# Kernel optimization log

Hardware: AMD Instinct MI355X
Metric: run time of the kernel (lower is better)

The kernel has to match this reference:

```python
import jax, jax.numpy as jnp
import numpy as np

H = 512      # hidden_size
FF = 4 * H   # expert FFN inner dim
E = 8        # expert_num
K = 2        # top_k
B, S = 4, 4096


def setup_inputs() -> dict:
    key = jax.random.key(0)
    ks = jax.random.split(key, 4)
    s = 0.02
    return {
        "x":  jax.random.normal(ks[0], (B, S, H), dtype=jnp.float32),
        "Wg": jax.random.normal(ks[1], (H, E), dtype=jnp.float32) * s,
        "bg": jnp.zeros((E,), dtype=jnp.float32),
        "W1": jax.random.normal(ks[2], (E, H, FF), dtype=jnp.float32) * s,
        "b1": jnp.zeros((E, FF), dtype=jnp.float32),
        "W2": jax.random.normal(ks[3], (E, FF, H), dtype=jnp.float32) * s,
        "b2": jnp.zeros((E, H), dtype=jnp.float32),
    }


def reference(x, Wg, bg, W1, b1, W2, b2):
    # gate + top-k routing
    logits = x @ Wg + bg                               # [B,S,E]
    w, idx = jax.lax.top_k(logits, K)                  # [B,S,K]
    w = jax.nn.softmax(w, axis=-1)                     # softmax over top-k logits

    # naive dense MoE: every expert runs on every token (matches torch source)
    h = jax.nn.silu(jnp.einsum('bsh,ehf->ebsf', x, W1) + b1[:, None, None, :])  # [E,B,S,FF]
    y = jnp.einsum('ebsf,efh->ebsh', h, W2) + b2[:, None, None, :]              # [E,B,S,H]

    # one-hot mask * top-k weight, combined over slots (same math as torch loop)
    comb = jnp.einsum('bske,bsk->ebs', jax.nn.one_hot(idx, E, dtype=x.dtype), w)  # [E,B,S]
    return jnp.einsum('ebsh,ebs->bsh', y, comb)        # [B,S,H]
```

## Files before the change

### kernel.cpp

```cpp
#include <hip/hip_runtime.h>
#include <hip/hip_bf16.h>
#include <math.h>


#define T_TOK 16384
#define H_DIM 512
#define FF_DIM 2048
#define E_NUM 8
#define NSLOT (T_TOK * 2)
#define NB_ROUTE 128

typedef __attribute__((ext_vector_type(4))) float f32x4;
typedef __attribute__((ext_vector_type(8))) short s16x8;

__device__ __forceinline__ void gload_lds16(const void* g, void* l) {
    __builtin_amdgcn_global_load_lds((const __attribute__((address_space(1))) void*)g,
                                     (__attribute__((address_space(3))) void*)l, 16, 0, 0);
}

__device__ __forceinline__ unsigned short f2bf(float f) {
    union { float f; unsigned int u; } a; a.f = f;
    unsigned int r = a.u + 0x7FFF + ((a.u >> 16) & 1);
    return (unsigned short)(r >> 16);
}


__global__ __launch_bounds__(256) void zero_f32(float* p, int n) {
    int i = (blockIdx.x * 256 + threadIdx.x) * 4;
    if (i < n) { f32x4 z = {0.f, 0.f, 0.f, 0.f}; *(f32x4*)(p + i) = z; }
}

__global__ __launch_bounds__(256) void convert_x_bf16(const float* __restrict__ x,
                                                      unsigned short* __restrict__ xb) {
    int i = (blockIdx.x * 256 + threadIdx.x) * 8;
    f32x4 a = *(const f32x4*)(x + i);
    f32x4 b = *(const f32x4*)(x + i + 4);
    s16x8 o;
    o[0] = (short)f2bf(a[0]); o[1] = (short)f2bf(a[1]);
    o[2] = (short)f2bf(a[2]); o[3] = (short)f2bf(a[3]);
    o[4] = (short)f2bf(b[0]); o[5] = (short)f2bf(b[1]);
    o[6] = (short)f2bf(b[2]); o[7] = (short)f2bf(b[3]);
    *(s16x8*)(xb + i) = o;
}

__global__ __launch_bounds__(256) void transpose_bf16(const float* __restrict__ src,
                                                      unsigned short* __restrict__ dst,
                                                      int R, int C) {
    const int e = blockIdx.z;
    const int c0 = blockIdx.x * 32, r0 = blockIdx.y * 32;
    __shared__ float tile[32][33];
    const float* s = src + (size_t)e * R * C;
    unsigned short* d = dst + (size_t)e * R * C;
    const int tid = threadIdx.x;
    for (int idx = tid; idx < 1024; idx += 256) {
        int r = idx >> 5, c = idx & 31;
        tile[r][c] = s[(size_t)(r0 + r) * C + c0 + c];
    }
    __syncthreads();
    for (int idx = tid; idx < 1024; idx += 256) {
        int r = idx >> 5, c = idx & 31;
        d[(size_t)(c0 + r) * R + r0 + c] = f2bf(tile[c][r]);
    }
}


__global__ __launch_bounds__(256) void gate_topk(const float* __restrict__ x,
                                                 const float* __restrict__ Wg,
                                                 const float* __restrict__ bg,
                                                 int* __restrict__ eidx,
                                                 float* __restrict__ ewt) {
    const int t = blockIdx.x * 4 + (threadIdx.x >> 6);
    const int l = threadIdx.x & 63;
    const float* xr = x + (size_t)t * H_DIM;
    double part[E_NUM];
#pragma unroll
    for (int e = 0; e < E_NUM; ++e) part[e] = 0.0;
#pragma unroll
    for (int i = 0; i < 8; ++i) {
        const int h = l + 64 * i;
        const double xv = (double)xr[h];
        const float* wr = Wg + (size_t)h * E_NUM;
#pragma unroll
        for (int e = 0; e < E_NUM; ++e) part[e] += xv * (double)wr[e];
    }
    for (int s = 1; s < 64; s <<= 1) {
#pragma unroll
        for (int e = 0; e < E_NUM; ++e) part[e] += __shfl_xor(part[e], s);
    }
    if (l == 0) {
        double lg[E_NUM];
#pragma unroll
        for (int e = 0; e < E_NUM; ++e) lg[e] = part[e] + (double)bg[e];
        int e0 = 0;
        for (int e = 1; e < E_NUM; ++e) if (lg[e] > lg[e0]) e0 = e;
        int e1 = (e0 == 0) ? 1 : 0;
        for (int e = 0; e < E_NUM; ++e) if (e != e0 && lg[e] > lg[e1]) e1 = e;
        double z = exp(lg[e1] - lg[e0]);
        float w0 = (float)(1.0 / (1.0 + z));
        float w1 = (float)(z / (1.0 + z));
        eidx[2 * t] = e0; eidx[2 * t + 1] = e1;
        ewt[2 * t] = w0; ewt[2 * t + 1] = w1;
    }
}


__global__ __launch_bounds__(256) void count_blocks(const int* __restrict__ eidx,
                                                    int* __restrict__ blockcnt) {
    __shared__ int cnt[E_NUM];
    if (threadIdx.x < E_NUM) cnt[threadIdx.x] = 0;
    __syncthreads();
    const int s = blockIdx.x * 256 + threadIdx.x;
    atomicAdd(&cnt[eidx[s]], 1);
    __syncthreads();
    if (threadIdx.x < E_NUM)
        blockcnt[blockIdx.x * E_NUM + threadIdx.x] = cnt[threadIdx.x];
}

__global__ __launch_bounds__(512) void scan_blocks(const int* __restrict__ blockcnt,
                                                   int* __restrict__ bbase,
                                                   int* __restrict__ offsets) {
    __shared__ int tot[E_NUM];
    __shared__ int obase[E_NUM + 1];
    const int e = threadIdx.x >> 6;
    const int l = threadIdx.x & 63;
    const int a = blockcnt[(2 * l) * E_NUM + e];
    const int b = blockcnt[(2 * l + 1) * E_NUM + e];
    const int s = a + b;
    int sc = s;
    for (int d = 1; d < 64; d <<= 1) {
        int o = __shfl_up(sc, d);
        if (l >= d) sc += o;
    }
    const int excl = sc - s;
    if (l == 63) tot[e] = sc;
    __syncthreads();
    if (threadIdx.x == 0) {
        int acc = 0;
        for (int i = 0; i < E_NUM; ++i) { obase[i] = acc; acc += tot[i]; }
        obase[E_NUM] = acc;
        for (int i = 0; i <= E_NUM; ++i) offsets[i] = obase[i];
    }
    __syncthreads();
    const int base = obase[e] + excl;
    bbase[(2 * l) * E_NUM + e] = base;
    bbase[(2 * l + 1) * E_NUM + e] = base + a;
}

__global__ __launch_bounds__(256) void scatter_slots(const int* __restrict__ eidx,
                                                     const float* __restrict__ ewt,
                                                     const int* __restrict__ bbase,
                                                     int* __restrict__ slot_token,
                                                     float* __restrict__ slot_w,
                                                     int* __restrict__ slot_of) {
    __shared__ int cur[E_NUM];
    if (threadIdx.x < E_NUM)
        cur[threadIdx.x] = bbase[blockIdx.x * E_NUM + threadIdx.x];
    __syncthreads();
    const int s = blockIdx.x * 256 + threadIdx.x;
    const int e = eidx[s];
    const int pos = atomicAdd(&cur[e], 1);
    slot_token[pos] = s >> 1;
    slot_w[pos] = ewt[s];
    slot_of[s] = pos;
}


template<int EPI, int NT, int KD, int NTOT, int MC, int LDA>
__global__ __launch_bounds__(256, 3) void ggemm(
    const unsigned short* __restrict__ Ag,
    const unsigned short* __restrict__ Bt,
    const float* __restrict__ bias,
    const int* __restrict__ slot_token,
    const float* __restrict__ slot_w,
    const int* __restrict__ offsets,
    unsigned short* __restrict__ Hout,
    float* __restrict__ out) {
    const int e = blockIdx.x;
    const int nt = blockIdx.y % NT;
    const int mc = blockIdx.y / NT;
    const int base = offsets[e];
    const int cnt = offsets[e + 1] - base;
    if (cnt == 0) return;
    const int n0 = nt * 128;

    __shared__ __align__(16) unsigned short Abuf[128 * 64];
    __shared__ __align__(16) unsigned short Bbuf[128 * 64];

    const int tid = threadIdx.x;
    const int w = tid >> 6;
    const int l = tid & 63;
    const int wm = (w & 1) << 6;
    const int wn = (w >> 1) << 6;

    int aoff[4], boff[4];
#pragma unroll
    for (int i = 0; i < 4; ++i) {
        int r = wm + i * 16 + (l & 15);
        aoff[i] = r * 128 + ((((l >> 4) ^ (r & 7))) << 4);
    }
#pragma unroll
    for (int j = 0; j < 4; ++j) {
        int r = wn + j * 16 + (l & 15);
        boff[j] = r * 128 + ((((l >> 4) ^ (r & 7))) << 4);
    }

    const int srow = tid >> 3;
    const int sce = (tid & 7) * 8;
    const unsigned short* Bg = Bt + (size_t)e * NTOT * KD + (size_t)n0 * KD;
    const int nk = KD / 64;

    int bsrc[4];
#pragma unroll
    for (int p = 0; p < 4; ++p) {
        int row = p * 32 + srow;
        bsrc[p] = (row & ~63) | ((row & 15) << 2) | ((row >> 4) & 3);
    }

    for (int m0 = mc * 128; m0 < cnt; m0 += MC * 128) {
        int tokr[4];
#pragma unroll
        for (int p = 0; p < 4; ++p) {
            int s = m0 + p * 32 + srow;
            if (s > cnt - 1) s = cnt - 1;
            tokr[p] = (EPI == 0) ? slot_token[base + s] : (base + s);
        }

        f32x4 acc[4][4] = {};
        for (int kt = 0; kt < nk; ++kt) {
            const int k0 = kt * 64;
            __syncthreads();
#pragma unroll
            for (int p = 0; p < 4; ++p) {
                int row = p * 32 + srow;
                int ce = sce ^ ((row & 7) * 8);
                gload_lds16(Ag + (size_t)tokr[p] * LDA + k0 + ce, &Abuf[row * 64 + sce]);
                gload_lds16(Bg + (size_t)bsrc[p] * KD + k0 + ce, &Bbuf[row * 64 + sce]);
            }
            __syncthreads();
            const char* Ab = (const char*)&Abuf[0];
            const char* Bb = (const char*)&Bbuf[0];
#pragma unroll
            for (int half = 0; half < 2; ++half) {
                const int kb = half << 6;
                s16x8 af[4], bfv[4];
#pragma unroll
                for (int i = 0; i < 4; ++i) af[i] = *(const s16x8*)(Ab + (aoff[i] ^ kb));
#pragma unroll
                for (int j = 0; j < 4; ++j) bfv[j] = *(const s16x8*)(Bb + (boff[j] ^ kb));
#pragma unroll
                for (int i = 0; i < 4; ++i)
#pragma unroll
                    for (int j = 0; j < 4; ++j)
                        acc[i][j] = __builtin_amdgcn_mfma_f32_16x16x32_bf16(af[i], bfv[j], acc[i][j], 0, 0, 0);
            }
        }

        const int c0 = wn + (l & 15) * 4;
        float b4[4];
#pragma unroll
        for (int j = 0; j < 4; ++j) b4[j] = bias[(size_t)e * NTOT + n0 + c0 + j];

#pragma unroll
        for (int i = 0; i < 4; ++i) {
            const int rb = wm + i * 16 + ((l >> 4) << 2);
#pragma unroll
            for (int r = 0; r < 4; ++r) {
                const int row = m0 + rb + r;
                if (row >= cnt) continue;
                const int slot = base + row;
                if (EPI == 0) {
                    float v0 = acc[i][0][r] + b4[0];
                    float v1 = acc[i][1][r] + b4[1];
                    float v2 = acc[i][2][r] + b4[2];
                    float v3 = acc[i][3][r] + b4[3];
                    v0 = v0 / (1.0f + __expf(-v0));
                    v1 = v1 / (1.0f + __expf(-v1));
                    v2 = v2 / (1.0f + __expf(-v2));
                    v3 = v3 / (1.0f + __expf(-v3));
                    uint2 pk;
                    pk.x = (unsigned int)f2bf(v0) | ((unsigned int)f2bf(v1) << 16);
                    pk.y = (unsigned int)f2bf(v2) | ((unsigned int)f2bf(v3) << 16);
                    *(uint2*)&Hout[(size_t)slot * NTOT + n0 + c0] = pk;
                } else if (EPI == 2) {
                    const float wgt = slot_w[slot];
                    f32x4 v;
#pragma unroll
                    for (int j = 0; j < 4; ++j) v[j] = wgt * (acc[i][j][r] + b4[j]);
                    *(f32x4*)&out[(size_t)slot * NTOT + n0 + c0] = v;
                } else {
                    const int tok = slot_token[slot];
                    const float wgt = slot_w[slot];
                    float* op = out + (size_t)tok * NTOT + n0 + c0;
#pragma unroll
                    for (int j = 0; j < 4; ++j)
                        atomicAdd(op + j, wgt * (acc[i][j][r] + b4[j]));
                }
            }
        }
    }
}

__global__ __launch_bounds__(256) void combine_y(const float* __restrict__ Y,
                                                 const int* __restrict__ slot_of,
                                                 float* __restrict__ out) {
    const int idx = blockIdx.x * 256 + threadIdx.x;
    const int t = idx >> 6;
    const int h = (idx & 63) * 8;
    const int sa = slot_of[2 * t];
    const int sb = slot_of[2 * t + 1];
    const float* pa = Y + (size_t)sa * H_DIM + h;
    const float* pb = Y + (size_t)sb * H_DIM + h;
    f32x4 a0 = *(const f32x4*)pa, a1 = *(const f32x4*)(pa + 4);
    f32x4 b0 = *(const f32x4*)pb, b1 = *(const f32x4*)(pb + 4);
    float* po = out + (size_t)t * H_DIM + h;
    *(f32x4*)po = a0 + b0;
    *(f32x4*)(po + 4) = a1 + b1;
}


extern "C" void kernel_launch(void* const* d_in, const int* in_sizes, int n_in,
                              void* d_out, int out_size, void* d_ws, size_t ws_size,
                              hipStream_t stream) {
    const float* x  = (const float*)d_in[0];
    const float* Wg = (const float*)d_in[1];
    const float* bg = (const float*)d_in[2];
    const float* W1 = (const float*)d_in[3];
    const float* b1 = (const float*)d_in[4];
    const float* W2 = (const float*)d_in[5];
    const float* b2 = (const float*)d_in[6];
    float* out = (float*)d_out;

    char* ws = (char*)d_ws;
    size_t off = 0;
    auto take = [&](size_t b) -> void* {
        void* p = ws + off;
        off = (off + b + 255) & ~(size_t)255;
        return p;
    };
    unsigned short* xb   = (unsigned short*)take((size_t)T_TOK * H_DIM * 2);
    unsigned short* W1t  = (unsigned short*)take((size_t)E_NUM * H_DIM * FF_DIM * 2);
    unsigned short* W2t  = (unsigned short*)take((size_t)E_NUM * H_DIM * FF_DIM * 2);
    int*   eidx       = (int*)take((size_t)T_TOK * 2 * 4);
    float* ewt        = (float*)take((size_t)T_TOK * 2 * 4);
    int*   slot_token = (int*)take((size_t)NSLOT * 4);
    float* slot_w     = (float*)take((size_t)NSLOT * 4);
    int*   slot_of    = (int*)take((size_t)NSLOT * 4);
    int*   blockcnt   = (int*)take((size_t)NB_ROUTE * E_NUM * 4);
    int*   bbase      = (int*)take((size_t)NB_ROUTE * E_NUM * 4);
    int*   offsets    = (int*)take(256);
    unsigned short* Hact = (unsigned short*)take((size_t)NSLOT * FF_DIM * 2);
    float* Yf = (float*)(ws + off);
    const int useY = (ws_size >= off + (size_t)NSLOT * H_DIM * 4) ? 1 : 0;

    convert_x_bf16<<<T_TOK * H_DIM / (256 * 8), 256, 0, stream>>>(x, xb);
    transpose_bf16<<<dim3(FF_DIM / 32, H_DIM / 32, E_NUM), 256, 0, stream>>>(W1, W1t, H_DIM, FF_DIM);
    transpose_bf16<<<dim3(H_DIM / 32, FF_DIM / 32, E_NUM), 256, 0, stream>>>(W2, W2t, FF_DIM, H_DIM);

    gate_topk<<<T_TOK / 4, 256, 0, stream>>>(x, Wg, bg, eidx, ewt);
    count_blocks<<<NB_ROUTE, 256, 0, stream>>>(eidx, blockcnt);
    scan_blocks<<<1, 512, 0, stream>>>(blockcnt, bbase, offsets);
    scatter_slots<<<NB_ROUTE, 256, 0, stream>>>(eidx, ewt, bbase, slot_token, slot_w, slot_of);

    ggemm<0, 16, 512, 2048, 8, 512><<<dim3(8, 128), 256, 0, stream>>>(
        xb, W1t, b1, slot_token, slot_w, offsets, Hact, out);
    if (useY) {
        ggemm<2, 4, 2048, 512, 32, 2048><<<dim3(8, 128), 256, 0, stream>>>(
            Hact, W2t, b2, slot_token, slot_w, offsets, Hact, Yf);
        combine_y<<<T_TOK * 64 / 256, 256, 0, stream>>>(Yf, slot_of, out);
    } else {
        zero_f32<<<(T_TOK * H_DIM / 4 + 255) / 256, 256, 0, stream>>>(out, T_TOK * H_DIM);
        ggemm<1, 4, 2048, 512, 32, 2048><<<dim3(8, 128), 256, 0, stream>>>(
            Hact, W2t, b2, slot_token, slot_w, offsets, Hact, out);
    }
    (void)in_sizes; (void)n_in; (void)out_size;
}
```

Before: 345.6 us.

## Double-buffer A tiles in LDS, load B fragments directly from global, fuse x conversion

The grouped GEMM no longer stages the weight (B) tile through LDS. Each lane loads its B fragments straight from global memory into registers, in the same permuted row order as before. The A tile is now double-buffered in LDS, with the next k-slice prefetched while the current one is consumed, so each k-step needs only one barrier. Separately, the fp32-to-bf16 conversion of x is folded into the gating kernel, which removes one launch and one extra read of x. The risks are exposed global-load latency and poorly coalesced, cache-dependent B reads, since B is not prefetched ahead of the MFMAs.

```diff
diff --git a/kernel.cpp b/kernel.cpp
--- a/kernel.cpp
+++ b/kernel.cpp
@@ -28,19 +28,6 @@
 __global__ __launch_bounds__(256) void zero_f32(float* p, int n) {
     int i = (blockIdx.x * 256 + threadIdx.x) * 4;
     if (i < n) { f32x4 z = {0.f, 0.f, 0.f, 0.f}; *(f32x4*)(p + i) = z; }
-}
-
-__global__ __launch_bounds__(256) void convert_x_bf16(const float* __restrict__ x,
-                                                      unsigned short* __restrict__ xb) {
-    int i = (blockIdx.x * 256 + threadIdx.x) * 8;
-    f32x4 a = *(const f32x4*)(x + i);
-    f32x4 b = *(const f32x4*)(x + i + 4);
-    s16x8 o;
-    o[0] = (short)f2bf(a[0]); o[1] = (short)f2bf(a[1]);
-    o[2] = (short)f2bf(a[2]); o[3] = (short)f2bf(a[3]);
-    o[4] = (short)f2bf(b[0]); o[5] = (short)f2bf(b[1]);
-    o[6] = (short)f2bf(b[2]); o[7] = (short)f2bf(b[3]);
-    *(s16x8*)(xb + i) = o;
 }
 
 __global__ __launch_bounds__(256) void transpose_bf16(const float* __restrict__ src,
@@ -68,20 +55,24 @@
                                                  const float* __restrict__ Wg,
                                                  const float* __restrict__ bg,
                                                  int* __restrict__ eidx,
-                                                 float* __restrict__ ewt) {
+                                                 float* __restrict__ ewt,
+                                                 unsigned short* __restrict__ xb) {
     const int t = blockIdx.x * 4 + (threadIdx.x >> 6);
     const int l = threadIdx.x & 63;
     const float* xr = x + (size_t)t * H_DIM;
+    unsigned short* xw = xb + (size_t)t * H_DIM;
     double part[E_NUM];
 #pragma unroll
     for (int e = 0; e < E_NUM; ++e) part[e] = 0.0;
 #pragma unroll
     for (int i = 0; i < 8; ++i) {
         const int h = l + 64 * i;
-        const double xv = (double)xr[h];
+        const float xv = xr[h];
+        xw[h] = f2bf(xv);
+        const double xd = (double)xv;
         const float* wr = Wg + (size_t)h * E_NUM;
 #pragma unroll
-        for (int e = 0; e < E_NUM; ++e) part[e] += xv * (double)wr[e];
+        for (int e = 0; e < E_NUM; ++e) part[e] += xd * (double)wr[e];
     }
     for (int s = 1; s < 64; s <<= 1) {
 #pragma unroll
@@ -183,8 +174,7 @@
     if (cnt == 0) return;
     const int n0 = nt * 128;
 
-    __shared__ __align__(16) unsigned short Abuf[128 * 64];
-    __shared__ __align__(16) unsigned short Bbuf[128 * 64];
+    __shared__ __align__(16) unsigned short Abuf[2][128 * 64];
 
     const int tid = threadIdx.x;
     const int w = tid >> 6;
@@ -192,29 +182,22 @@
     const int wm = (w & 1) << 6;
     const int wn = (w >> 1) << 6;
 
-    int aoff[4], boff[4];
+    int aoff[4];
 #pragma unroll
     for (int i = 0; i < 4; ++i) {
         int r = wm + i * 16 + (l & 15);
         aoff[i] = r * 128 + ((((l >> 4) ^ (r & 7))) << 4);
     }
-#pragma unroll
-    for (int j = 0; j < 4; ++j) {
-        int r = wn + j * 16 + (l & 15);
-        boff[j] = r * 128 + ((((l >> 4) ^ (r & 7))) << 4);
-    }
+
+    const unsigned short* Brow[4];
+#pragma unroll
+    for (int j = 0; j < 4; ++j)
+        Brow[j] = Bt + (size_t)e * NTOT * KD
+                     + (size_t)(n0 + wn + (l & 15) * 4 + j) * KD + ((l >> 4) * 8);
 
     const int srow = tid >> 3;
     const int sce = (tid & 7) * 8;
-    const unsigned short* Bg = Bt + (size_t)e * NTOT * KD + (size_t)n0 * KD;
     const int nk = KD / 64;
-
-    int bsrc[4];
-#pragma unroll
-    for (int p = 0; p < 4; ++p) {
-        int row = p * 32 + srow;
-        bsrc[p] = (row & ~63) | ((row & 15) << 2) | ((row >> 4) & 3);
-    }
 
     for (int m0 = mc * 128; m0 < cnt; m0 += MC * 128) {
         int tokr[4];
@@ -224,34 +207,47 @@
             if (s > cnt - 1) s = cnt - 1;
             tokr[p] = (EPI == 0) ? slot_token[base + s] : (base + s);
         }
+#pragma unroll
+        for (int p = 0; p < 4; ++p) {
+            int row = p * 32 + srow;
+            int ce = sce ^ ((row & 7) * 8);
+            gload_lds16(Ag + (size_t)tokr[p] * LDA + ce, &Abuf[0][row * 64 + sce]);
+        }
 
         f32x4 acc[4][4] = {};
         for (int kt = 0; kt < nk; ++kt) {
-            const int k0 = kt * 64;
+            const int cur = kt & 1;
             __syncthreads();
-#pragma unroll
-            for (int p = 0; p < 4; ++p) {
-                int row = p * 32 + srow;
-                int ce = sce ^ ((row & 7) * 8);
-                gload_lds16(Ag + (size_t)tokr[p] * LDA + k0 + ce, &Abuf[row * 64 + sce]);
-                gload_lds16(Bg + (size_t)bsrc[p] * KD + k0 + ce, &Bbuf[row * 64 + sce]);
+            if (kt + 1 < nk) {
+                const int k0 = (kt + 1) * 64;
+#pragma unroll
+                for (int p = 0; p < 4; ++p) {
+                    int row = p * 32 + srow;
+                    int ce = sce ^ ((row & 7) * 8);
+                    gload_lds16(Ag + (size_t)tokr[p] * LDA + k0 + ce,
+                                &Abuf[cur ^ 1][row * 64 + sce]);
+                }
             }
-            __syncthreads();
-            const char* Ab = (const char*)&Abuf[0];
-            const char* Bb = (const char*)&Bbuf[0];
+            s16x8 bfv[2][4];
+#pragma unroll
+            for (int half = 0; half < 2; ++half)
+#pragma unroll
+                for (int j = 0; j < 4; ++j)
+                    bfv[half][j] = *(const s16x8*)(Brow[j] + kt * 64 + half * 32);
+
+            const char* Ab = (const char*)&Abuf[cur][0];
 #pragma unroll
             for (int half = 0; half < 2; ++half) {
                 const int kb = half << 6;
-                s16x8 af[4], bfv[4];
+                s16x8 af[4];
 #pragma unroll
                 for (int i = 0; i < 4; ++i) af[i] = *(const s16x8*)(Ab + (aoff[i] ^ kb));
 #pragma unroll
-                for (int j = 0; j < 4; ++j) bfv[j] = *(const s16x8*)(Bb + (boff[j] ^ kb));
-#pragma unroll
                 for (int i = 0; i < 4; ++i)
 #pragma unroll
                     for (int j = 0; j < 4; ++j)
-                        acc[i][j] = __builtin_amdgcn_mfma_f32_16x16x32_bf16(af[i], bfv[j], acc[i][j], 0, 0, 0);
+                        acc[i][j] = __builtin_amdgcn_mfma_f32_16x16x32_bf16(
+                            af[i], bfv[half][j], acc[i][j], 0, 0, 0);
             }
         }
 
@@ -297,6 +293,7 @@
                 }
             }
         }
+        __syncthreads();
     }
 }
 
@@ -352,11 +349,10 @@
     float* Yf = (float*)(ws + off);
     const int useY = (ws_size >= off + (size_t)NSLOT * H_DIM * 4) ? 1 : 0;
 
-    convert_x_bf16<<<T_TOK * H_DIM / (256 * 8), 256, 0, stream>>>(x, xb);
     transpose_bf16<<<dim3(FF_DIM / 32, H_DIM / 32, E_NUM), 256, 0, stream>>>(W1, W1t, H_DIM, FF_DIM);
     transpose_bf16<<<dim3(H_DIM / 32, FF_DIM / 32, E_NUM), 256, 0, stream>>>(W2, W2t, FF_DIM, H_DIM);
 
-    gate_topk<<<T_TOK / 4, 256, 0, stream>>>(x, Wg, bg, eidx, ewt);
+    gate_topk<<<T_TOK / 4, 256, 0, stream>>>(x, Wg, bg, eidx, ewt, xb);
     count_blocks<<<NB_ROUTE, 256, 0, stream>>>(eidx, blockcnt);
     scan_blocks<<<1, 512, 0, stream>>>(blockcnt, bbase, offsets);
     scatter_slots<<<NB_ROUTE, 256, 0, stream>>>(eidx, ewt, bbase, slot_token, slot_w, slot_of);
```

Measured after the change: 582.3 us. 68.5% more time.
